# Kernel tuning notes

Measured on AMD Instinct MI355X. Metric: run time of the kernel, lower is better.

Reference implementation:

```python
import jax, jax.numpy as jnp
import numpy as np

H, W = 160, 480
C_IMG = 256
VFC = [64, 128, 256]
N_PTS = 120000


def setup_inputs() -> dict:
    key = jax.random.key(0)
    ks = jax.random.split(key, 16)
    inp = {}
    inp["img_feat"] = jax.random.normal(ks[0], (C_IMG, H, W), jnp.float32)
    inp["seg_prob"] = jax.random.uniform(ks[1], (1, 2, H, W), jnp.float32)
    for i, c in enumerate(VFC):
        inp[f"voxel_feat{i}"] = jax.random.normal(ks[2 + i], (N_PTS, c), jnp.float32)
        x = jax.random.randint(ks[5 + i], (N_PTS,), 0, W + 1)  # col coord in [0, W]
        y = jax.random.randint(ks[8 + i], (N_PTS,), 0, H + 1)  # row coord in [0, H]
        inp[f"img_grid{i}"] = jnp.stack([x, y], axis=1).astype(jnp.int32)
    inp["red_w0"] = jax.random.normal(ks[11], (VFC[2], VFC[0]), jnp.float32) * 0.05
    inp["red_b0"] = jnp.zeros((VFC[2],), jnp.float32)
    inp["red_w1"] = jax.random.normal(ks[12], (VFC[2], VFC[1]), jnp.float32) * 0.05
    inp["red_b1"] = jnp.zeros((VFC[2],), jnp.float32)
    inp["sb_w"] = jax.random.normal(ks[13], (1, C_IMG + VFC[2], 3, 3), jnp.float32) * 0.02
    inp["sb_b"] = jnp.zeros((1,), jnp.float32)
    return inp


def pts2img(coor, pts_feat):
    # coor: [N,2] int (x, y); torch does coor[:, [1,0]] then grid[y, x] = feat
    c = pts_feat.shape[1]
    grid = jnp.zeros((H + 1, W + 1, c), pts_feat.dtype)
    grid = grid.at[coor[:, 1], coor[:, 0]].set(pts_feat, mode="drop")
    return grid[:-1, :-1].transpose(2, 0, 1)  # [C, H, W]


def reference(img_feat, seg_prob, voxel_feat0, voxel_feat1, voxel_feat2,
              img_grid0, img_grid1, img_grid2,
              red_w0, red_b0, red_w1, red_b1, sb_w, sb_b):
    # seg-gated image features
    enhanced = img_feat * seg_prob[0, 1][None]  # [C_IMG, H, W]

    # level 0: scatter + 1x1 conv (64 -> 256)
    p0 = pts2img(img_grid0, voxel_feat0)
    p0 = jnp.einsum('chw,oc->ohw', p0, red_w0) + red_b0[:, None, None]
    # level 1: scatter + 1x1 conv (128 -> 256)
    p1 = pts2img(img_grid1, voxel_feat1)
    p1 = jnp.einsum('chw,oc->ohw', p1, red_w1) + red_b1[:, None, None]
    # level 2: scatter only (already 256)
    p2 = pts2img(img_grid2, voxel_feat2)
    pt_img = p0 + p1 + p2  # [256, H, W]

    fused = jnp.concatenate([enhanced, pt_img], axis=0)[None]  # [1, 512, H, W]
    conv = jax.lax.conv_general_dilated(
        fused, sb_w, window_strides=(1, 1), padding='SAME',
        dimension_numbers=('NCHW', 'OIHW', 'NCHW'))
    conv = conv + sb_b[None, :, None, None]
    attention_map = jax.nn.sigmoid(conv[0])  # [1, H, W]
    return enhanced * attention_map
```

## Files before the change

### kernel.cpp

```cpp
#include <hip/hip_runtime.h>
#include <math.h>

#define H 160
#define W 480
#define HW 76800
#define NPTS 120000
#define NUNIT 6

#define OFF_W1M 307200
#define OFF_W2M 614400
#define OFF_T9  921600
#define OFF_WE0 17510400
#define OFF_WE1 17513472
#define OFF_BC  17519616

__global__ __launch_bounds__(256) void prep_and_scatter(
    const float* __restrict__ rw0, const float* __restrict__ rw1,
    const float* __restrict__ rb0, const float* __restrict__ rb1,
    const float* __restrict__ sbw,
    float* __restrict__ Weff0, float* __restrict__ Weff1, float* __restrict__ bconst,
    const int2* __restrict__ g0, const int2* __restrict__ g1, const int2* __restrict__ g2,
    int* __restrict__ w0, int* __restrict__ w1, int* __restrict__ w2) {
  if (blockIdx.x < 7) {
    int t = blockIdx.x * 256 + threadIdx.x;
    if (t < 576) {
      int jj = t / 64, k = t % 64;
      float s = 0.f;
      for (int c = 0; c < 256; ++c) s = fmaf(rw0[c * 64 + k], sbw[(256 + c) * 9 + jj], s);
      Weff0[k * 12 + jj] = s;
    } else if (t < 1728) {
      int tt = t - 576;
      int jj = tt / 128, k = tt % 128;
      float s = 0.f;
      for (int c = 0; c < 256; ++c) s = fmaf(rw1[c * 128 + k], sbw[(256 + c) * 9 + jj], s);
      Weff1[k * 12 + jj] = s;
    } else if (t < 1737) {
      int jj = t - 1728;
      float s = 0.f;
      for (int c = 0; c < 256; ++c) s = fmaf(rb0[c] + rb1[c], sbw[(256 + c) * 9 + jj], s);
      bconst[jj] = s;
    }
  } else {
    int j = (blockIdx.x - 7) * 256 + threadIdx.x;
    if (j >= NPTS) return;
    int2 c;
    c = g0[j];
    if ((unsigned)c.x < W && (unsigned)c.y < H) atomicMax(&w0[c.y * W + c.x], j);
    c = g1[j];
    if ((unsigned)c.x < W && (unsigned)c.y < H) atomicMax(&w1[c.y * W + c.x], j);
    c = g2[j];
    if ((unsigned)c.x < W && (unsigned)c.y < H) atomicMax(&w2[c.y * W + c.x], j);
  }
}

template <int NF4>
__device__ __forceinline__ void ld_batch(const float4* __restrict__ r, float4* v) {
#pragma unroll
  for (int i = 0; i < NF4; ++i) v[i] = r[i];
}

template <int NF4, int WS>
__device__ __forceinline__ void fma_batch(const float4* v, const float* __restrict__ wbase,
                                          float acc[9]) {
#pragma unroll
  for (int i = 0; i < NF4; ++i) {
    const float* wc = wbase + i * 4 * WS;
#pragma unroll
    for (int j = 0; j < 9; ++j) {
      acc[j] = fmaf(v[i].x, wc[j], acc[j]);
      acc[j] = fmaf(v[i].y, wc[WS + j], acc[j]);
      acc[j] = fmaf(v[i].z, wc[2 * WS + j], acc[j]);
      acc[j] = fmaf(v[i].w, wc[3 * WS + j], acc[j]);
    }
  }
}

__global__ __launch_bounds__(256, 3) void t9_kernel(
    const float* __restrict__ img, const float* __restrict__ seg,
    const float* __restrict__ vf0, const float* __restrict__ vf1,
    const float* __restrict__ vf2,
    const int* __restrict__ w0m, const int* __restrict__ w1m,
    const int* __restrict__ w2m,
    const float* __restrict__ We0, const float* __restrict__ We1,
    const float* __restrict__ sbw, float* __restrict__ t9) {
  int p = blockIdx.x * 256 + threadIdx.x;
  int u = blockIdx.y;
  float acc[9];
#pragma unroll
  for (int j = 0; j < 9; ++j) acc[j] = 0.f;

  if (u < 2) {
    const int c0 = u * 128;
    float s = seg[HW + p];
    for (int cc = 0; cc < 128; cc += 16) {
      float v[16];
#pragma unroll
      for (int t = 0; t < 16; ++t) v[t] = img[(size_t)(c0 + cc + t) * HW + p];
      __builtin_amdgcn_sched_barrier(0);
#pragma unroll
      for (int t = 0; t < 16; ++t) {
        const float* wr = sbw + (c0 + cc + t) * 9;
#pragma unroll
        for (int j = 0; j < 9; ++j) acc[j] = fmaf(v[t], wr[j], acc[j]);
      }
    }
#pragma unroll
    for (int j = 0; j < 9; ++j) acc[j] *= s;
  } else if (u == 2) {
    int w0 = w0m[p], w1 = w1m[p];
    const float4* r0 = (const float4*)(vf0 + (size_t)(w0 < 0 ? 0 : w0) * 64);
    const float4* r1 = (const float4*)(vf1 + (size_t)(w1 < 0 ? 0 : w1) * 128);
    float4 v0[16], v1[12];
    ld_batch<16>(r0, v0);
    ld_batch<12>(r1, v1);
    __builtin_amdgcn_sched_barrier(0);
    if (w0 >= 0) fma_batch<16, 12>(v0, We0, acc);
    if (w1 >= 0) fma_batch<12, 12>(v1, We1, acc);
  } else if (u == 3) {
    int w1 = w1m[p], w2 = w2m[p];
    const float4* r1 = (const float4*)(vf1 + (size_t)(w1 < 0 ? 0 : w1) * 128 + 48);
    const float4* r2 = (const float4*)(vf2 + (size_t)(w2 < 0 ? 0 : w2) * 256);
    float4 v1[20], v2[8];
    ld_batch<20>(r1, v1);
    ld_batch<8>(r2, v2);
    __builtin_amdgcn_sched_barrier(0);
    if (w1 >= 0) fma_batch<20, 12>(v1, We1 + 48 * 12, acc);
    if (w2 >= 0) fma_batch<8, 9>(v2, sbw + 256 * 9, acc);
  } else {
    int cbase = (u == 4) ? 32 : 144;
    int w2 = w2m[p];
    const float4* r2 = (const float4*)(vf2 + (size_t)(w2 < 0 ? 0 : w2) * 256 + cbase);
    float4 v2[28];
    ld_batch<28>(r2, v2);
    __builtin_amdgcn_sched_barrier(0);
    if (w2 >= 0) fma_batch<28, 9>(v2, sbw + (256 + cbase) * 9, acc);
  }

  float* dst = t9 + (size_t)u * 9 * HW + p;
#pragma unroll
  for (int j = 0; j < 9; ++j) dst[(size_t)j * HW] = acc[j];
}

__global__ __launch_bounds__(256) void conv_sig_kernel(
    const float* __restrict__ t9, const float* __restrict__ bconst,
    const float* __restrict__ sbb, const float* __restrict__ seg,
    float* __restrict__ sa) {
  int p = blockIdx.x * blockDim.x + threadIdx.x;
  int y = p / W, x = p - y * W;
  float s = sbb[0];
#pragma unroll
  for (int dy = -1; dy <= 1; ++dy) {
#pragma unroll
    for (int dx = -1; dx <= 1; ++dx) {
      int yy = y + dy, xx = x + dx;
      if ((unsigned)yy < H && (unsigned)xx < W) {
        int j = (dy + 1) * 3 + (dx + 1);
        int q = yy * W + xx;
        float t = bconst[j];
#pragma unroll
        for (int u = 0; u < NUNIT; ++u) t += t9[(size_t)(u * 9 + j) * HW + q];
        s += t;
      }
    }
  }
  float att = 1.f / (1.f + expf(-s));
  sa[p] = att * seg[HW + p];
}

__global__ __launch_bounds__(256) void final_mul_kernel(
    const float* __restrict__ img, const float* __restrict__ sa, float* __restrict__ out) {
  int i = blockIdx.x * blockDim.x + threadIdx.x;
  int e = i * 4;
  int p = e % HW;
  float4 v = *(const float4*)(img + e);
  float4 g = *(const float4*)(sa + p);
  float4 o = make_float4(v.x * g.x, v.y * g.y, v.z * g.z, v.w * g.w);
  *(float4*)(out + e) = o;
}

extern "C" void kernel_launch(void* const* d_in, const int* in_sizes, int n_in,
                              void* d_out, int out_size, void* d_ws, size_t ws_size,
                              hipStream_t stream) {
  const float* img = (const float*)d_in[0];
  const float* seg = (const float*)d_in[1];
  int iV0 = 2, iG0 = 3, iV1 = 4, iG1 = 5, iV2 = 6, iG2 = 7;
  if (in_sizes[3] != 2 * NPTS) {
    iV0 = 2; iV1 = 3; iV2 = 4; iG0 = 5; iG1 = 6; iG2 = 7;
  }
  const float* vf0 = (const float*)d_in[iV0];
  const float* vf1 = (const float*)d_in[iV1];
  const float* vf2 = (const float*)d_in[iV2];
  const int2* g0 = (const int2*)d_in[iG0];
  const int2* g1 = (const int2*)d_in[iG1];
  const int2* g2 = (const int2*)d_in[iG2];
  const float* rw0 = (const float*)d_in[8];
  const float* rb0 = (const float*)d_in[9];
  const float* rw1 = (const float*)d_in[10];
  const float* rb1 = (const float*)d_in[11];
  const float* sbw = (const float*)d_in[12];
  const float* sbb = (const float*)d_in[13];

  char* ws = (char*)d_ws;
  int* w0m = (int*)(ws + 0);
  int* w1m = (int*)(ws + OFF_W1M);
  int* w2m = (int*)(ws + OFF_W2M);
  float* t9 = (float*)(ws + OFF_T9);
  float* Weff0 = (float*)(ws + OFF_WE0);
  float* Weff1 = (float*)(ws + OFF_WE1);
  float* bconst = (float*)(ws + OFF_BC);
  float* sa = (float*)(ws + 0);

  float* out = (float*)d_out;

  hipMemsetAsync(w0m, 0xFF, 3 * 307200, stream);
  prep_and_scatter<<<7 + (NPTS + 255) / 256, 256, 0, stream>>>(
      rw0, rw1, rb0, rb1, sbw, Weff0, Weff1, bconst, g0, g1, g2, w0m, w1m, w2m);
  dim3 tg(HW / 256, NUNIT);
  t9_kernel<<<tg, 256, 0, stream>>>(img, seg, vf0, vf1, vf2, w0m, w1m, w2m,
                                    Weff0, Weff1, sbw, t9);
  conv_sig_kernel<<<HW / 256, 256, 0, stream>>>(t9, bconst, sbb, seg, sa);
  final_mul_kernel<<<(out_size / 4) / 256, 256, 0, stream>>>(img, sa, out);
}
```

Baseline: 368.6 us.

## Stage scattered voxel-row gathers through LDS via global_load_lds chunks

The register-batched float4 gathers of voxel feature rows are replaced with direct global-to-LDS loads (`global_load_lds`, 16 bytes per lane) into a per-wave staging buffer. Each row is processed in chunks of up to 8 float4, with an explicit wait on outstanding memory operations before the FMAs read the chunk back from LDS. The min-blocks-per-CU launch bound is dropped. The aim is to cut VGPR pressure from holding up to 28 float4 per thread, which should allow higher occupancy. The cost is fewer loads in flight per thread, a serialising wait per chunk, and extra LDS traffic.

```diff
diff --git a/kernel.cpp b/kernel.cpp
--- a/kernel.cpp
+++ b/kernel.cpp
@@ -53,29 +53,36 @@
   }
 }
 
-template <int NF4>
-__device__ __forceinline__ void ld_batch(const float4* __restrict__ r, float4* v) {
-#pragma unroll
-  for (int i = 0; i < NF4; ++i) v[i] = r[i];
-}
-
-template <int NF4, int WS>
-__device__ __forceinline__ void fma_batch(const float4* v, const float* __restrict__ wbase,
-                                          float acc[9]) {
-#pragma unroll
-  for (int i = 0; i < NF4; ++i) {
-    const float* wc = wbase + i * 4 * WS;
-#pragma unroll
-    for (int j = 0; j < 9; ++j) {
-      acc[j] = fmaf(v[i].x, wc[j], acc[j]);
-      acc[j] = fmaf(v[i].y, wc[WS + j], acc[j]);
-      acc[j] = fmaf(v[i].z, wc[2 * WS + j], acc[j]);
-      acc[j] = fmaf(v[i].w, wc[3 * WS + j], acc[j]);
-    }
-  }
-}
-
-__global__ __launch_bounds__(256, 3) void t9_kernel(
+__device__ __forceinline__ void glds16(const float* g, float* l) {
+  __builtin_amdgcn_global_load_lds(
+      (const __attribute__((address_space(1))) void*)g,
+      (__attribute__((address_space(3))) void*)l, 16, 0, 0);
+}
+
+template <int NG, int WS>
+__device__ __forceinline__ void seg_lds(const float4* row, const float* __restrict__ wbase,
+                                        bool act, int lane, float* buf, float acc[9]) {
+#pragma unroll
+  for (int k = 0; k < NG; ++k) glds16((const float*)(row + k), buf + k * 256);
+  asm volatile("s_waitcnt vmcnt(0)" ::: "memory");
+  __builtin_amdgcn_sched_barrier(0);
+  if (act) {
+#pragma unroll
+    for (int k = 0; k < NG; ++k) {
+      float4 v = *(const float4*)(buf + k * 256 + lane * 4);
+      const float* wc = wbase + 4 * k * WS;
+#pragma unroll
+      for (int j = 0; j < 9; ++j) {
+        acc[j] = fmaf(v.x, wc[j], acc[j]);
+        acc[j] = fmaf(v.y, wc[WS + j], acc[j]);
+        acc[j] = fmaf(v.z, wc[2 * WS + j], acc[j]);
+        acc[j] = fmaf(v.w, wc[3 * WS + j], acc[j]);
+      }
+    }
+  }
+}
+
+__global__ __launch_bounds__(256) void t9_kernel(
     const float* __restrict__ img, const float* __restrict__ seg,
     const float* __restrict__ vf0, const float* __restrict__ vf1,
     const float* __restrict__ vf2,
@@ -83,8 +90,11 @@
     const int* __restrict__ w2m,
     const float* __restrict__ We0, const float* __restrict__ We1,
     const float* __restrict__ sbw, float* __restrict__ t9) {
+  __shared__ float stg[4][2048];
   int p = blockIdx.x * 256 + threadIdx.x;
   int u = blockIdx.y;
+  int lane = threadIdx.x & 63;
+  float* buf = stg[threadIdx.x >> 6];
   float acc[9];
 #pragma unroll
   for (int j = 0; j < 9; ++j) acc[j] = 0.f;
@@ -110,30 +120,28 @@
     int w0 = w0m[p], w1 = w1m[p];
     const float4* r0 = (const float4*)(vf0 + (size_t)(w0 < 0 ? 0 : w0) * 64);
     const float4* r1 = (const float4*)(vf1 + (size_t)(w1 < 0 ? 0 : w1) * 128);
-    float4 v0[16], v1[12];
-    ld_batch<16>(r0, v0);
-    ld_batch<12>(r1, v1);
-    __builtin_amdgcn_sched_barrier(0);
-    if (w0 >= 0) fma_batch<16, 12>(v0, We0, acc);
-    if (w1 >= 0) fma_batch<12, 12>(v1, We1, acc);
+    seg_lds<8, 12>(r0, We0, w0 >= 0, lane, buf, acc);
+    seg_lds<8, 12>(r0 + 8, We0 + 32 * 12, w0 >= 0, lane, buf, acc);
+    seg_lds<8, 12>(r1, We1, w1 >= 0, lane, buf, acc);
+    seg_lds<4, 12>(r1 + 8, We1 + 32 * 12, w1 >= 0, lane, buf, acc);
   } else if (u == 3) {
     int w1 = w1m[p], w2 = w2m[p];
     const float4* r1 = (const float4*)(vf1 + (size_t)(w1 < 0 ? 0 : w1) * 128 + 48);
     const float4* r2 = (const float4*)(vf2 + (size_t)(w2 < 0 ? 0 : w2) * 256);
-    float4 v1[20], v2[8];
-    ld_batch<20>(r1, v1);
-    ld_batch<8>(r2, v2);
-    __builtin_amdgcn_sched_barrier(0);
-    if (w1 >= 0) fma_batch<20, 12>(v1, We1 + 48 * 12, acc);
-    if (w2 >= 0) fma_batch<8, 9>(v2, sbw + 256 * 9, acc);
+    seg_lds<8, 12>(r1, We1 + 48 * 12, w1 >= 0, lane, buf, acc);
+    seg_lds<8, 12>(r1 + 8, We1 + 80 * 12, w1 >= 0, lane, buf, acc);
+    seg_lds<4, 12>(r1 + 16, We1 + 112 * 12, w1 >= 0, lane, buf, acc);
+    seg_lds<8, 9>(r2, sbw + 256 * 9, w2 >= 0, lane, buf, acc);
   } else {
     int cbase = (u == 4) ? 32 : 144;
     int w2 = w2m[p];
     const float4* r2 = (const float4*)(vf2 + (size_t)(w2 < 0 ? 0 : w2) * 256 + cbase);
-    float4 v2[28];
-    ld_batch<28>(r2, v2);
-    __builtin_amdgcn_sched_barrier(0);
-    if (w2 >= 0) fma_batch<28, 9>(v2, sbw + (256 + cbase) * 9, acc);
+    const float* wb = sbw + (256 + cbase) * 9;
+    bool act = (w2 >= 0);
+    seg_lds<8, 9>(r2, wb, act, lane, buf, acc);
+    seg_lds<8, 9>(r2 + 8, wb + 32 * 9, act, lane, buf, acc);
+    seg_lds<8, 9>(r2 + 16, wb + 64 * 9, act, lane, buf, acc);
+    seg_lds<4, 9>(r2 + 24, wb + 96 * 9, act, lane, buf, acc);
   }
 
   float* dst = t9 + (size_t)u * 9 * HW + p;
```

Measured after the change: 368.1 us. No clear change (-0.1%).

## Iterate over winning points instead of pixels and atomically accumulate tap partials

Applied to the files above, without the earlier changes.

The per-pixel gather over scatter-winner maps is replaced by a per-point pass: each point checks whether it won its cell, and 16-lane groups cooperatively dot its feature row with the projected weights, reduce via shuffles, and atomically add 9 tap values into one shared 9xHW buffer. Image channel blocks also atomically add into the same buffer, so the conv kernel reads 9 planes instead of 54. This removes reads for empty pixels and the large t9 intermediate, but adds float atomics (nondeterministic summation order), an extra memset, and a grid sized by NPTS that wastes image-path blocks beyond HW.

```diff
diff --git a/kernel.cpp b/kernel.cpp
--- a/kernel.cpp
+++ b/kernel.cpp
@@ -5,14 +5,13 @@
 #define W 480
 #define HW 76800
 #define NPTS 120000
-#define NUNIT 6
 
 #define OFF_W1M 307200
 #define OFF_W2M 614400
-#define OFF_T9  921600
-#define OFF_WE0 17510400
-#define OFF_WE1 17513472
-#define OFF_BC  17519616
+#define OFF_ACC 921600
+#define OFF_WE0 3686400
+#define OFF_WE1 3689472
+#define OFF_BC  3695616
 
 __global__ __launch_bounds__(256) void prep_and_scatter(
     const float* __restrict__ rw0, const float* __restrict__ rw1,
@@ -53,45 +52,22 @@
   }
 }
 
-template <int NF4>
-__device__ __forceinline__ void ld_batch(const float4* __restrict__ r, float4* v) {
-#pragma unroll
-  for (int i = 0; i < NF4; ++i) v[i] = r[i];
-}
-
-template <int NF4, int WS>
-__device__ __forceinline__ void fma_batch(const float4* v, const float* __restrict__ wbase,
-                                          float acc[9]) {
-#pragma unroll
-  for (int i = 0; i < NF4; ++i) {
-    const float* wc = wbase + i * 4 * WS;
-#pragma unroll
-    for (int j = 0; j < 9; ++j) {
-      acc[j] = fmaf(v[i].x, wc[j], acc[j]);
-      acc[j] = fmaf(v[i].y, wc[WS + j], acc[j]);
-      acc[j] = fmaf(v[i].z, wc[2 * WS + j], acc[j]);
-      acc[j] = fmaf(v[i].w, wc[3 * WS + j], acc[j]);
-    }
-  }
-}
-
-__global__ __launch_bounds__(256, 3) void t9_kernel(
+__global__ __launch_bounds__(256) void fused_t9(
     const float* __restrict__ img, const float* __restrict__ seg,
     const float* __restrict__ vf0, const float* __restrict__ vf1,
     const float* __restrict__ vf2,
-    const int* __restrict__ w0m, const int* __restrict__ w1m,
-    const int* __restrict__ w2m,
+    const int2* __restrict__ g0, const int2* __restrict__ g1, const int2* __restrict__ g2,
+    const int* __restrict__ w0m, const int* __restrict__ w1m, const int* __restrict__ w2m,
     const float* __restrict__ We0, const float* __restrict__ We1,
-    const float* __restrict__ sbw, float* __restrict__ t9) {
-  int p = blockIdx.x * 256 + threadIdx.x;
+    const float* __restrict__ sbw, float* __restrict__ accum) {
   int u = blockIdx.y;
-  float acc[9];
-#pragma unroll
-  for (int j = 0; j < 9; ++j) acc[j] = 0.f;
-
   if (u < 2) {
+    int p = blockIdx.x * 256 + threadIdx.x;
+    if (p >= HW) return;
     const int c0 = u * 128;
-    float s = seg[HW + p];
+    float acc[9];
+#pragma unroll
+    for (int j = 0; j < 9; ++j) acc[j] = 0.f;
     for (int cc = 0; cc < 128; cc += 16) {
       float v[16];
 #pragma unroll
@@ -104,45 +80,92 @@
         for (int j = 0; j < 9; ++j) acc[j] = fmaf(v[t], wr[j], acc[j]);
       }
     }
-#pragma unroll
-    for (int j = 0; j < 9; ++j) acc[j] *= s;
-  } else if (u == 2) {
-    int w0 = w0m[p], w1 = w1m[p];
-    const float4* r0 = (const float4*)(vf0 + (size_t)(w0 < 0 ? 0 : w0) * 64);
-    const float4* r1 = (const float4*)(vf1 + (size_t)(w1 < 0 ? 0 : w1) * 128);
-    float4 v0[16], v1[12];
-    ld_batch<16>(r0, v0);
-    ld_batch<12>(r1, v1);
-    __builtin_amdgcn_sched_barrier(0);
-    if (w0 >= 0) fma_batch<16, 12>(v0, We0, acc);
-    if (w1 >= 0) fma_batch<12, 12>(v1, We1, acc);
-  } else if (u == 3) {
-    int w1 = w1m[p], w2 = w2m[p];
-    const float4* r1 = (const float4*)(vf1 + (size_t)(w1 < 0 ? 0 : w1) * 128 + 48);
-    const float4* r2 = (const float4*)(vf2 + (size_t)(w2 < 0 ? 0 : w2) * 256);
-    float4 v1[20], v2[8];
-    ld_batch<20>(r1, v1);
-    ld_batch<8>(r2, v2);
-    __builtin_amdgcn_sched_barrier(0);
-    if (w1 >= 0) fma_batch<20, 12>(v1, We1 + 48 * 12, acc);
-    if (w2 >= 0) fma_batch<8, 9>(v2, sbw + 256 * 9, acc);
-  } else {
-    int cbase = (u == 4) ? 32 : 144;
-    int w2 = w2m[p];
-    const float4* r2 = (const float4*)(vf2 + (size_t)(w2 < 0 ? 0 : w2) * 256 + cbase);
-    float4 v2[28];
-    ld_batch<28>(r2, v2);
-    __builtin_amdgcn_sched_barrier(0);
-    if (w2 >= 0) fma_batch<28, 9>(v2, sbw + (256 + cbase) * 9, acc);
-  }
-
-  float* dst = t9 + (size_t)u * 9 * HW + p;
-#pragma unroll
-  for (int j = 0; j < 9; ++j) dst[(size_t)j * HW] = acc[j];
+    float s = seg[HW + p];
+#pragma unroll
+    for (int j = 0; j < 9; ++j) atomicAdd(&accum[(size_t)j * HW + p], acc[j] * s);
+    return;
+  }
+
+  int lvl = u - 2;
+  int jp = blockIdx.x * 256 + threadIdx.x;
+  int lane = threadIdx.x & 63;
+  int wg = lane >> 4, sub = lane & 15;
+  const int2* g = (lvl == 0) ? g0 : (lvl == 1) ? g1 : g2;
+  const int* wm = (lvl == 0) ? w0m : (lvl == 1) ? w1m : w2m;
+
+  int valid = 0, cell = 0;
+  if (jp < NPTS) {
+    int2 c = g[jp];
+    if ((unsigned)c.x < W && (unsigned)c.y < H) {
+      cell = c.y * W + c.x;
+      valid = (wm[cell] == jp) ? 1 : 0;
+    }
+  }
+  unsigned long long m = __ballot(valid != 0);
+
+  for (int s = 0; s < 16; ++s) {
+    if (((m >> (s * 4)) & 0xFull) == 0) continue;
+    int cl = s * 4 + wg;
+    int vj = __shfl(jp, cl);
+    int vcell = __shfl(cell, cl);
+    int vvalid = __shfl(valid, cl);
+    if (vvalid) {
+      float acc[9];
+#pragma unroll
+      for (int j = 0; j < 9; ++j) acc[j] = 0.f;
+      if (lvl == 0) {
+        float4 v = ((const float4*)(vf0 + (size_t)vj * 64))[sub];
+        const float* wc = We0 + sub * 4 * 12;
+#pragma unroll
+        for (int j = 0; j < 9; ++j) {
+          acc[j] = fmaf(v.x, wc[j], acc[j]);
+          acc[j] = fmaf(v.y, wc[12 + j], acc[j]);
+          acc[j] = fmaf(v.z, wc[24 + j], acc[j]);
+          acc[j] = fmaf(v.w, wc[36 + j], acc[j]);
+        }
+      } else if (lvl == 1) {
+#pragma unroll
+        for (int ch = 0; ch < 2; ++ch) {
+          float4 v = ((const float4*)(vf1 + (size_t)vj * 128))[sub + 16 * ch];
+          const float* wc = We1 + (sub * 4 + 64 * ch) * 12;
+#pragma unroll
+          for (int j = 0; j < 9; ++j) {
+            acc[j] = fmaf(v.x, wc[j], acc[j]);
+            acc[j] = fmaf(v.y, wc[12 + j], acc[j]);
+            acc[j] = fmaf(v.z, wc[24 + j], acc[j]);
+            acc[j] = fmaf(v.w, wc[36 + j], acc[j]);
+          }
+        }
+      } else {
+#pragma unroll
+        for (int ch = 0; ch < 4; ++ch) {
+          float4 v = ((const float4*)(vf2 + (size_t)vj * 256))[sub + 16 * ch];
+          const float* wc = sbw + (256 + sub * 4 + 64 * ch) * 9;
+#pragma unroll
+          for (int j = 0; j < 9; ++j) {
+            acc[j] = fmaf(v.x, wc[j], acc[j]);
+            acc[j] = fmaf(v.y, wc[9 + j], acc[j]);
+            acc[j] = fmaf(v.z, wc[18 + j], acc[j]);
+            acc[j] = fmaf(v.w, wc[27 + j], acc[j]);
+          }
+        }
+      }
+#pragma unroll
+      for (int d = 1; d < 16; d <<= 1) {
+#pragma unroll
+        for (int j = 0; j < 9; ++j) acc[j] += __shfl_xor(acc[j], d);
+      }
+      if (sub == 0) {
+#pragma unroll
+        for (int j = 0; j < 9; ++j)
+          atomicAdd(&accum[(size_t)j * HW + vcell], acc[j]);
+      }
+    }
+  }
 }
 
 __global__ __launch_bounds__(256) void conv_sig_kernel(
-    const float* __restrict__ t9, const float* __restrict__ bconst,
+    const float* __restrict__ accum, const float* __restrict__ bconst,
     const float* __restrict__ sbb, const float* __restrict__ seg,
     float* __restrict__ sa) {
   int p = blockIdx.x * blockDim.x + threadIdx.x;
@@ -156,10 +179,7 @@
       if ((unsigned)yy < H && (unsigned)xx < W) {
         int j = (dy + 1) * 3 + (dx + 1);
         int q = yy * W + xx;
-        float t = bconst[j];
-#pragma unroll
-        for (int u = 0; u < NUNIT; ++u) t += t9[(size_t)(u * 9 + j) * HW + q];
-        s += t;
+        s += bconst[j] + accum[(size_t)j * HW + q];
       }
     }
   }
@@ -204,7 +224,7 @@
   int* w0m = (int*)(ws + 0);
   int* w1m = (int*)(ws + OFF_W1M);
   int* w2m = (int*)(ws + OFF_W2M);
-  float* t9 = (float*)(ws + OFF_T9);
+  float* accum = (float*)(ws + OFF_ACC);
   float* Weff0 = (float*)(ws + OFF_WE0);
   float* Weff1 = (float*)(ws + OFF_WE1);
   float* bconst = (float*)(ws + OFF_BC);
@@ -213,11 +233,12 @@
   float* out = (float*)d_out;
 
   hipMemsetAsync(w0m, 0xFF, 3 * 307200, stream);
+  hipMemsetAsync(accum, 0, 9 * HW * 4, stream);
   prep_and_scatter<<<7 + (NPTS + 255) / 256, 256, 0, stream>>>(
       rw0, rw1, rb0, rb1, sbw, Weff0, Weff1, bconst, g0, g1, g2, w0m, w1m, w2m);
-  dim3 tg(HW / 256, NUNIT);
-  t9_kernel<<<tg, 256, 0, stream>>>(img, seg, vf0, vf1, vf2, w0m, w1m, w2m,
-                                    Weff0, Weff1, sbw, t9);
-  conv_sig_kernel<<<HW / 256, 256, 0, stream>>>(t9, bconst, sbb, seg, sa);
+  dim3 tg((NPTS + 255) / 256, 5);
+  fused_t9<<<tg, 256, 0, stream>>>(img, seg, vf0, vf1, vf2, g0, g1, g2,
+                                   w0m, w1m, w2m, Weff0, Weff1, sbw, accum);
+  conv_sig_kernel<<<HW / 256, 256, 0, stream>>>(accum, bconst, sbb, seg, sa);
   final_mul_kernel<<<(out_size / 4) / 256, 256, 0, stream>>>(img, sa, out);
 }
```

New measurement: 481.4 us. +30.6%, slower.
